# Performance work log

Hardware: AMD Instinct MI355X
Metric: run time of the kernel (lower is better)

The kernel has to match this reference:

```python
import jax, jax.numpy as jnp
import numpy as np

VOCAB = 4096
CODE_DIM = 3
DECAY = 0.99
EPS = 1e-05


def setup_inputs() -> dict:
    key = jax.random.key(0)
    k1, k2, k3, k4 = jax.random.split(key, 4)
    feats = jax.random.normal(k1, (4, 8192, CODE_DIM), dtype=jnp.float32)
    embed = jax.random.normal(k2, (VOCAB, CODE_DIM), dtype=jnp.float32)
    ema_cluster_size = jax.random.uniform(k3, (VOCAB,), dtype=jnp.float32)
    ema_weight = jax.random.normal(k4, (VOCAB, CODE_DIM), dtype=jnp.float32)
    return {"feats": feats, "embed": embed,
            "ema_cluster_size": ema_cluster_size, "ema_weight": ema_weight}


def reference(feats, embed, ema_cluster_size, ema_weight):
    B, L, D = feats.shape
    flat = feats.reshape(-1, D)  # (N, D)
    # squared-euclidean distances to all codes: (N, V)
    dist = (jnp.sum(flat * flat, axis=1, keepdims=True)
            - 2.0 * flat @ embed.T
            + jnp.sum(embed * embed, axis=1))
    idx = jnp.argmin(dist, axis=1)  # (N,)
    quant = embed[idx].reshape(B, L, D)

    # EMA codebook update (training mode), done with segment_sum instead of a
    # dense (N, V) one-hot matmul -- same math.
    counts = jax.ops.segment_sum(jnp.ones_like(flat[:, 0]), idx, num_segments=VOCAB)
    sums = jax.ops.segment_sum(flat, idx, num_segments=VOCAB)  # (V, D)
    new_cluster_size = DECAY * ema_cluster_size + (1.0 - DECAY) * counts
    new_ema_weight = DECAY * ema_weight + (1.0 - DECAY) * sums
    n = jnp.sum(new_cluster_size)
    cluster_size = (new_cluster_size + EPS) / (n + VOCAB * EPS) * n
    new_embed = new_ema_weight / cluster_size[:, None]

    # VQ loss with stop-gradients matching torch detach semantics
    loss = (jnp.mean((quant - jax.lax.stop_gradient(feats)) ** 2)
            + 0.25 * jnp.mean((feats - jax.lax.stop_gradient(quant)) ** 2))
    # straight-through estimator
    quant_st = feats + jax.lax.stop_gradient(quant - feats)
    return (quant_st, idx.reshape(B, L), loss,
            new_cluster_size, new_ema_weight, new_embed)
```

## Files before the change

kernel.cpp:

```cpp
#include <hip/hip_runtime.h>
#include <math.h>

#pragma clang fp contract(off)

#define VOCAB 4096
#define NPTS  32768
#define NELEM 98304
#define BLOCK 1024
#define NWAVE 16
#define CPW   (VOCAB / NWAVE)
#define PPL   2
#define PTS_PER_BLOCK (64 * PPL)

__global__ __launch_bounds__(BLOCK) void vq_assign(
    const float* __restrict__ feats, const float* __restrict__ embed,
    float* __restrict__ out_quant, float* __restrict__ out_idx,
    float* __restrict__ counts, float* __restrict__ sums,
    float* __restrict__ sse)
{
  extern __shared__ float4 codes[];
  __shared__ float dbuf[NWAVE][PPL][64];
  __shared__ int   ibuf[NWAVE][PPL][64];

  const int tid  = threadIdx.x;
  const int lane = tid & 63;
  const int wv   = tid >> 6;

  for (int c = tid; c < VOCAB; c += BLOCK) {
    float e0 = embed[3 * c + 0];
    float e1 = embed[3 * c + 1];
    float e2 = embed[3 * c + 2];
    float esq = (e0 * e0 + e1 * e1) + e2 * e2;
    codes[c] = make_float4(e0, e1, e2, esq);
  }
  __syncthreads();

  const int pbase = blockIdx.x * PTS_PER_BLOCK;
  float px[PPL][3], xsq[PPL];
  #pragma unroll
  for (int s = 0; s < PPL; ++s) {
    const int p = pbase + s * 64 + lane;
    px[s][0] = feats[3 * p + 0];
    px[s][1] = feats[3 * p + 1];
    px[s][2] = feats[3 * p + 2];
    xsq[s] = (px[s][0] * px[s][0] + px[s][1] * px[s][1]) + px[s][2] * px[s][2];
  }

  float best[PPL] = {INFINITY, INFINITY};
  int   bidx[PPL] = {0, 0};
  const float4* wc = codes + wv * CPW;
  const int cbase = wv * CPW;

  #pragma unroll 16
  for (int k = 0; k < CPW; ++k) {
    float4 e = wc[k];
    #pragma unroll
    for (int s = 0; s < PPL; ++s) {
      float dot = fmaf(px[s][2], e.z, fmaf(px[s][1], e.y, px[s][0] * e.x));
      float d = (xsq[s] - 2.0f * dot) + e.w;
      if (d < best[s]) { best[s] = d; bidx[s] = cbase + k; }
    }
  }

  #pragma unroll
  for (int s = 0; s < PPL; ++s) {
    dbuf[wv][s][lane] = best[s];
    ibuf[wv][s][lane] = bidx[s];
  }
  __syncthreads();

  if (wv == 0) {
    #pragma unroll
    for (int s = 0; s < PPL; ++s) {
      float b = best[s];
      int   bi = bidx[s];
      #pragma unroll
      for (int w = 1; w < NWAVE; ++w) {
        float od = dbuf[w][s][lane];
        int   oi = ibuf[w][s][lane];
        if (od < b || (od == b && oi < bi)) { b = od; bi = oi; }
      }

      const int p = pbase + s * 64 + lane;
      const float4 q = codes[bi];
      const float x0 = px[s][0], x1 = px[s][1], x2 = px[s][2];

      out_quant[3 * p + 0] = x0 + (q.x - x0);
      out_quant[3 * p + 1] = x1 + (q.y - x1);
      out_quant[3 * p + 2] = x2 + (q.z - x2);
      out_idx[p] = (float)bi;

      atomicAdd(&counts[bi], 1.0f);
      atomicAdd(&sums[3 * bi + 0], x0);
      atomicAdd(&sums[3 * bi + 1], x1);
      atomicAdd(&sums[3 * bi + 2], x2);

      float d0 = q.x - x0, d1 = q.y - x1, d2 = q.z - x2;
      float l = (d0 * d0 + d1 * d1) + d2 * d2;
      #pragma unroll
      for (int m = 1; m <= 32; m <<= 1) l += __shfl_xor(l, m, 64);
      if (lane == 0) atomicAdd(sse, l);
    }
  }
}

__global__ __launch_bounds__(1024) void vq_ema(
    const float* __restrict__ counts, const float* __restrict__ sums,
    const float* __restrict__ sse,
    const float* __restrict__ ema_cs, const float* __restrict__ ema_w,
    float* __restrict__ out_loss, float* __restrict__ out_ncs,
    float* __restrict__ out_nw, float* __restrict__ out_nemb)
{
  __shared__ float part[16];
  const int tid = threadIdx.x;
  const float DEC = 0.99f;
  const float OMD = (float)(1.0 - 0.99);
  const float EPS = 1e-5f;

  float ncs[4];
  float nw[12];
  float nsum = 0.0f;

  #pragma unroll
  for (int k = 0; k < 4; ++k) {
    int v = k * 1024 + tid;
    float t = DEC * ema_cs[v] + OMD * counts[v];
    ncs[k] = t;
    out_ncs[v] = t;
    nsum += t;
    #pragma unroll
    for (int d = 0; d < 3; ++d) {
      float w = DEC * ema_w[3 * v + d] + OMD * sums[3 * v + d];
      nw[3 * k + d] = w;
      out_nw[3 * v + d] = w;
    }
  }

  #pragma unroll
  for (int m = 1; m <= 32; m <<= 1) nsum += __shfl_xor(nsum, m, 64);
  if ((tid & 63) == 0) part[tid >> 6] = nsum;
  __syncthreads();

  float n = 0.0f;
  #pragma unroll
  for (int i = 0; i < 16; ++i) n += part[i];
  const float denom = n + (float)VOCAB * EPS;

  #pragma unroll
  for (int k = 0; k < 4; ++k) {
    int v = k * 1024 + tid;
    float cs = (ncs[k] + EPS) / denom * n;
    #pragma unroll
    for (int d = 0; d < 3; ++d)
      out_nemb[3 * v + d] = nw[3 * k + d] / cs;
  }

  if (tid == 0) {
    float m = sse[0] / (float)NELEM;
    out_loss[0] = m + 0.25f * m;
  }
}

extern "C" void kernel_launch(void* const* d_in, const int* in_sizes, int n_in,
                              void* d_out, int out_size, void* d_ws, size_t ws_size,
                              hipStream_t stream) {
  const float* feats  = (const float*)d_in[0];
  const float* embed  = (const float*)d_in[1];
  const float* ema_cs = (const float*)d_in[2];
  const float* ema_w  = (const float*)d_in[3];

  float* out      = (float*)d_out;
  float* o_quant  = out;
  float* o_idx    = out + 98304;
  float* o_loss   = out + 131072;
  float* o_ncs    = out + 131073;
  float* o_nw     = out + 135169;
  float* o_nemb   = out + 147457;

  float* ws_counts = (float*)d_ws;
  float* ws_sums   = ws_counts + VOCAB;
  float* ws_sse    = ws_sums + 3 * VOCAB;

  hipMemsetAsync(d_ws, 0, (size_t)(VOCAB * 4 + 1) * sizeof(float), stream);

  vq_assign<<<NPTS / PTS_PER_BLOCK, BLOCK, VOCAB * sizeof(float4), stream>>>(
      feats, embed, o_quant, o_idx, ws_counts, ws_sums, ws_sse);

  vq_ema<<<1, 1024, 0, stream>>>(
      ws_counts, ws_sums, ws_sse, ema_cs, ema_w,
      o_loss, o_ncs, o_nw, o_nemb);
}
```

Before: 50.33 us.

## Precompute doubled codebook in prep kernel and split code reads between LDS and global

Adds a prep kernel that packs the codebook into float4 entries holding the doubled coordinates and the squared norm, so the assign kernel copies them into LDS instead of recomputing them. The distance loop drops the multiply by 2. The inner loop now reads even codes from LDS and odd codes straight from global memory through a vector-register base pointer, spreading load traffic across the LDS and vector-memory paths. Launch bounds ask for 4 waves per SIMD. This costs an extra kernel launch and relies on L1/L2 hits for the global code reads; the quantized output is rescaled by 0.5, which can round differently from the original.

```diff
diff --git a/kernel.cpp b/kernel.cpp
--- a/kernel.cpp
+++ b/kernel.cpp
@@ -12,8 +12,19 @@
 #define PPL   2
 #define PTS_PER_BLOCK (64 * PPL)
 
-__global__ __launch_bounds__(BLOCK) void vq_assign(
-    const float* __restrict__ feats, const float* __restrict__ embed,
+__global__ __launch_bounds__(1024) void vq_prep(
+    const float* __restrict__ embed, float4* __restrict__ gcodes)
+{
+  const int c = blockIdx.x * 1024 + threadIdx.x;
+  float e0 = embed[3 * c + 0];
+  float e1 = embed[3 * c + 1];
+  float e2 = embed[3 * c + 2];
+  float esq = (e0 * e0 + e1 * e1) + e2 * e2;
+  gcodes[c] = make_float4(e0 + e0, e1 + e1, e2 + e2, esq);
+}
+
+__global__ __launch_bounds__(BLOCK, 4) void vq_assign(
+    const float* __restrict__ feats, const float4* __restrict__ gcodes,
     float* __restrict__ out_quant, float* __restrict__ out_idx,
     float* __restrict__ counts, float* __restrict__ sums,
     float* __restrict__ sse)
@@ -26,13 +37,8 @@
   const int lane = tid & 63;
   const int wv   = tid >> 6;
 
-  for (int c = tid; c < VOCAB; c += BLOCK) {
-    float e0 = embed[3 * c + 0];
-    float e1 = embed[3 * c + 1];
-    float e2 = embed[3 * c + 2];
-    float esq = (e0 * e0 + e1 * e1) + e2 * e2;
-    codes[c] = make_float4(e0, e1, e2, esq);
-  }
+  #pragma unroll
+  for (int c = tid; c < VOCAB; c += BLOCK) codes[c] = gcodes[c];
   __syncthreads();
 
   const int pbase = blockIdx.x * PTS_PER_BLOCK;
@@ -48,17 +54,25 @@
 
   float best[PPL] = {INFINITY, INFINITY};
   int   bidx[PPL] = {0, 0};
-  const float4* wc = codes + wv * CPW;
+
   const int cbase = wv * CPW;
-
-  #pragma unroll 16
-  for (int k = 0; k < CPW; ++k) {
-    float4 e = wc[k];
+  const float4* lc = codes + cbase;
+  int vz;
+  asm volatile("v_mov_b32 %0, 0" : "=v"(vz));
+  const float4* gcv = gcodes + cbase + vz;
+
+  #pragma unroll 8
+  for (int k = 0; k < CPW; k += 2) {
+    float4 eL = lc[k];
+    float4 eG = gcv[k + 1];
     #pragma unroll
     for (int s = 0; s < PPL; ++s) {
-      float dot = fmaf(px[s][2], e.z, fmaf(px[s][1], e.y, px[s][0] * e.x));
-      float d = (xsq[s] - 2.0f * dot) + e.w;
-      if (d < best[s]) { best[s] = d; bidx[s] = cbase + k; }
+      float dotL = fmaf(px[s][2], eL.z, fmaf(px[s][1], eL.y, px[s][0] * eL.x));
+      float dL = (xsq[s] - dotL) + eL.w;
+      if (dL < best[s]) { best[s] = dL; bidx[s] = cbase + k; }
+      float dotG = fmaf(px[s][2], eG.z, fmaf(px[s][1], eG.y, px[s][0] * eG.x));
+      float dG = (xsq[s] - dotG) + eG.w;
+      if (dG < best[s]) { best[s] = dG; bidx[s] = cbase + k + 1; }
     }
   }
 
@@ -83,11 +97,14 @@
 
       const int p = pbase + s * 64 + lane;
       const float4 q = codes[bi];
+      const float q0 = 0.5f * q.x;
+      const float q1 = 0.5f * q.y;
+      const float q2 = 0.5f * q.z;
       const float x0 = px[s][0], x1 = px[s][1], x2 = px[s][2];
 
-      out_quant[3 * p + 0] = x0 + (q.x - x0);
-      out_quant[3 * p + 1] = x1 + (q.y - x1);
-      out_quant[3 * p + 2] = x2 + (q.z - x2);
+      out_quant[3 * p + 0] = x0 + (q0 - x0);
+      out_quant[3 * p + 1] = x1 + (q1 - x1);
+      out_quant[3 * p + 2] = x2 + (q2 - x2);
       out_idx[p] = (float)bi;
 
       atomicAdd(&counts[bi], 1.0f);
@@ -95,7 +112,7 @@
       atomicAdd(&sums[3 * bi + 1], x1);
       atomicAdd(&sums[3 * bi + 2], x2);
 
-      float d0 = q.x - x0, d1 = q.y - x1, d2 = q.z - x2;
+      float d0 = q0 - x0, d1 = q1 - x1, d2 = q2 - x2;
       float l = (d0 * d0 + d1 * d1) + d2 * d2;
       #pragma unroll
       for (int m = 1; m <= 32; m <<= 1) l += __shfl_xor(l, m, 64);
@@ -180,11 +197,14 @@
   float* ws_counts = (float*)d_ws;
   float* ws_sums   = ws_counts + VOCAB;
   float* ws_sse    = ws_sums + 3 * VOCAB;
+  float4* ws_gcodes = (float4*)((float*)d_ws + 16400);
 
   hipMemsetAsync(d_ws, 0, (size_t)(VOCAB * 4 + 1) * sizeof(float), stream);
 
+  vq_prep<<<VOCAB / 1024, 1024, 0, stream>>>(embed, ws_gcodes);
+
   vq_assign<<<NPTS / PTS_PER_BLOCK, BLOCK, VOCAB * sizeof(float4), stream>>>(
-      feats, embed, o_quant, o_idx, ws_counts, ws_sums, ws_sse);
+      feats, ws_gcodes, o_quant, o_idx, ws_counts, ws_sums, ws_sse);
 
   vq_ema<<<1, 1024, 0, stream>>>(
       ws_counts, ws_sums, ws_sse, ema_cs, ema_w,
```

After: 51.05 us. Within noise of the previous version (+1.4%).
